# Performance work log

Hardware: AMD Instinct MI355X
Metric: run time of the kernel (lower is better)

Reference implementation:

```python
import jax, jax.numpy as jnp
import numpy as np

V, D, H, F, L, SMAX = 32000, 768, 12, 3072, 6, 512
DN = D // H
NEG = -1e9
EPS = 1e-5


def _pos_encoding(S, d, dtype):
    # pe[pos,2i]   = sin(pos / 10000**(2i/d))
    # pe[pos,2i+1] = cos(pos / 10000**(2(i+1)/d))   (note the i+1, as in source)
    pos = jnp.arange(S, dtype=jnp.float32)[:, None]
    i = jnp.arange(d // 2, dtype=jnp.float32)[None, :]
    pe_sin = jnp.sin(pos / jnp.power(10000.0, 2.0 * i / d))
    pe_cos = jnp.cos(pos / jnp.power(10000.0, 2.0 * (i + 1.0) / d))
    pe = jnp.zeros((S, d), jnp.float32)
    pe = pe.at[:, 0::2].set(pe_sin).at[:, 1::2].set(pe_cos)
    return pe.astype(dtype)


def _layernorm(z, g, b):
    m = jnp.mean(z, axis=-1, keepdims=True)
    v = jnp.mean(jnp.square(z - m), axis=-1, keepdims=True)
    return (z - m) * jax.lax.rsqrt(v + EPS) * g + b


def setup_inputs() -> dict:
    key = jax.random.key(0)
    ks = jax.random.split(key, 20)
    s = 0.02
    inp = {
        "x": jax.random.randint(ks[0], (16, 512), 0, V, dtype=jnp.int64 if jax.config.read("jax_enable_x64") else jnp.int32),
        "padding_mask": jax.random.randint(ks[1], (16, 512, 512), 0, 2, dtype=jnp.int32),
        "emb": jax.random.normal(ks[2], (V, D), jnp.float32) * s,
        # per-head separate projections, stacked: [L, H, D, DN]
        "Wq": jax.random.normal(ks[3], (L, H, D, DN), jnp.float32) * s,
        "bq": jnp.zeros((L, H, DN), jnp.float32),
        "Wk": jax.random.normal(ks[4], (L, H, D, DN), jnp.float32) * s,
        "bk": jnp.zeros((L, H, DN), jnp.float32),
        "Wv": jax.random.normal(ks[5], (L, H, D, DN), jnp.float32) * s,
        "bv": jnp.zeros((L, H, DN), jnp.float32),
        "Wo": jax.random.normal(ks[6], (L, D, D), jnp.float32) * s,
        "bo": jnp.zeros((L, D), jnp.float32),
        "W1": jax.random.normal(ks[7], (L, D, F), jnp.float32) * s,
        "b1": jnp.zeros((L, F), jnp.float32),
        "W2": jax.random.normal(ks[8], (L, F, D), jnp.float32) * s,
        "b2": jnp.zeros((L, D), jnp.float32),
        "g1": jnp.ones((L, D), jnp.float32),
        "be1": jnp.zeros((L, D), jnp.float32),
        "g2": jnp.ones((L, D), jnp.float32),
        "be2": jnp.zeros((L, D), jnp.float32),
    }
    return inp


def reference(x, padding_mask, emb, Wq, bq, Wk, bk, Wv, bv, Wo, bo,
              W1, b1, W2, b2, g1, be1, g2, be2):
    B, S = x.shape
    h = emb[x]                                   # [B,S,D]
    h = h + _pos_encoding(S, D, h.dtype)[None]   # dropout is identity in eval
    bias = padding_mask.astype(h.dtype)[:, None] * NEG   # [B,1,S,S]
    scale = 1.0 / np.sqrt(DN)
    for l in range(L):
        q = jnp.einsum("bsd,hde->bhse", h, Wq[l]) + bq[l][None, :, None, :]
        k = jnp.einsum("bsd,hde->bhse", h, Wk[l]) + bk[l][None, :, None, :]
        v = jnp.einsum("bsd,hde->bhse", h, Wv[l]) + bv[l][None, :, None, :]
        scores = jnp.einsum("bhse,bhte->bhst", q, k) * scale + bias
        attn = jax.nn.softmax(scores, axis=-1)
        o = jnp.einsum("bhst,bhte->bhse", attn, v)        # [B,H,S,DN]
        o = o.transpose(0, 2, 1, 3).reshape(B, S, D)      # concat heads
        o = o @ Wo[l] + bo[l]
        h = _layernorm(h + o, g1[l], be1[l])
        ff = jax.nn.relu(h @ W1[l] + b1[l]) @ W2[l] + b2[l]
        h = _layernorm(h + ff, g2[l], be2[l])
    return h
```

## Files before the change

### kernel.cpp

```cpp
#include <hip/hip_runtime.h>
#include <hip/hip_bf16.h>
#include <math.h>

#define B_  16
#define S_  512
#define D_  768
#define H_  12
#define DN_ 64
#define F_  3072
#define L_  6
#define T_  (B_*S_)
#define QKVN 2304
#define TDC ((size_t)T_*D_)

typedef unsigned short ushort_t;
typedef short short8 __attribute__((ext_vector_type(8)));
typedef float floatx4 __attribute__((ext_vector_type(4)));

#define LDS_AS(p) ((__attribute__((address_space(3))) void*)(p))
#define GLB_AS(p) ((const __attribute__((address_space(1))) void*)(p))

static __device__ __forceinline__ float b2f(ushort_t u) {
  union { unsigned int i; float f; } x; x.i = ((unsigned int)u) << 16; return x.f;
}
static __device__ __forceinline__ ushort_t f2b(float f) {
  union { float f; unsigned int i; } x; x.f = f;
  unsigned int r = x.i + 0x7fffu + ((x.i >> 16) & 1u);
  return (ushort_t)(r >> 16);
}

__global__ __launch_bounds__(64) void probe_x(const int* __restrict__ x,
                                              int* __restrict__ xstride) {
  if (threadIdx.x == 0) {
    int allzero = 1;
    for (int i = 0; i < 64; ++i) allzero &= (x[2 * i + 1] == 0) ? 1 : 0;
    *xstride = allzero ? 2 : 1;
  }
}

__global__ __launch_bounds__(256) void pe_kernel(float* __restrict__ pe) {
  const int s = blockIdx.x;
  const float pos = (float)s;
  for (int d = threadIdx.x; d < D_; d += 256) {
    float v;
    if ((d & 1) == 0) {
      float freq = powf(10000.0f, -(float)d * (1.0f / 768.0f));
      v = sinf(pos * freq);
    } else {
      float freq = powf(10000.0f, -(float)(d + 1) * (1.0f / 768.0f));
      v = cosf(pos * freq);
    }
    pe[(size_t)s * D_ + d] = v;
  }
}

__global__ __launch_bounds__(256) void embed_pe(const int* __restrict__ x,
                                                const int* __restrict__ xstride,
                                                const float* __restrict__ emb,
                                                const float* __restrict__ pe,
                                                float* __restrict__ h32,
                                                ushort_t* __restrict__ h16) {
  const int t = blockIdx.x;
  const int s = t & (S_ - 1);
  const int tok = x[t * (*xstride)];
  const float* ep = emb + (size_t)tok * D_;
  const float* pp = pe + (size_t)s * D_;
  for (int d = threadIdx.x; d < D_; d += 256) {
    float v = ep[d] + pp[d];
    h32[(size_t)t * D_ + d] = v;
    h16[(size_t)t * D_ + d] = f2b(v);
  }
}

__global__ __launch_bounds__(256) void mask_bits(const int* __restrict__ mask,
                                                 unsigned long long* __restrict__ bits) {
  const int gw = (blockIdx.x * 256 + threadIdx.x) >> 6;
  const int lane = threadIdx.x & 63;
  const int m = mask[(size_t)gw * 64 + lane];
  unsigned long long bal = __ballot(m != 0);
  if (lane == 0) bits[gw] = bal;
}

__global__ __launch_bounds__(256) void pack_bias(const float* __restrict__ bq,
                                                 const float* __restrict__ bk,
                                                 const float* __restrict__ bv,
                                                 float* __restrict__ bqkv) {
  const int i = blockIdx.x * 256 + threadIdx.x;
  if (i < L_ * D_) {
    const int l = i / D_, c = i - l * D_;
    bqkv[(size_t)l * QKVN + c]          = bq[i];
    bqkv[(size_t)l * QKVN + 768 + c]    = bk[i];
    bqkv[(size_t)l * QKVN + 1536 + c]   = bv[i];
  }
}

__global__ __launch_bounds__(256) void transpose_cast(const float* __restrict__ in,
                                                      ushort_t* __restrict__ out,
                                                      int R, int C, int ZH,
                                                      size_t strideL, size_t strideH) {
  __shared__ float tb[32][33];
  const int c0 = blockIdx.x * 32, r0 = blockIdx.y * 32;
  const int z = blockIdx.z;
  const float* ib = in + (size_t)z * R * C;
  ushort_t* ob = out + (size_t)(z / ZH) * strideL + (size_t)(z % ZH) * strideH;
  const int i = threadIdx.x >> 5;
  const int j = threadIdx.x & 31;
  #pragma unroll
  for (int t = 0; t < 4; ++t)
    tb[i + 8 * t][j] = ib[(size_t)(r0 + i + 8 * t) * C + c0 + j];
  __syncthreads();
  #pragma unroll
  for (int t = 0; t < 4; ++t)
    ob[(size_t)(c0 + i + 8 * t) * R + r0 + j] = f2b(tb[j][i + 8 * t]);
}

__global__ __launch_bounds__(256) void transpose_v(const ushort_t* __restrict__ qkv,
                                                   ushort_t* __restrict__ vT) {
  __shared__ ushort_t tb[32][33];
  const int s0 = blockIdx.x * 32, e0 = blockIdx.y * 32;
  const int bh = blockIdx.z;
  const int b = bh / 12, hh = bh - b * 12;
  const int i = threadIdx.x >> 5, j = threadIdx.x & 31;
  #pragma unroll
  for (int t = 0; t < 4; ++t)
    tb[i + 8 * t][j] = qkv[((size_t)(b * S_ + s0 + i + 8 * t)) * QKVN + 1536 + hh * 64 + e0 + j];
  __syncthreads();
  #pragma unroll
  for (int t = 0; t < 4; ++t)
    vT[((size_t)(bh * 64 + e0 + i + 8 * t)) * S_ + s0 + j] = tb[j][i + 8 * t];
}

template<int RELU>
__global__ __launch_bounds__(256) void gemm_mfma(const ushort_t* __restrict__ A,
                                                 const ushort_t* __restrict__ Bt,
                                                 const float* __restrict__ bias,
                                                 ushort_t* __restrict__ C,
                                                 int N, int K) {
  __shared__ ushort_t Alds[128 * 64];
  __shared__ ushort_t Blds[128 * 64];
  const int tid = threadIdx.x;
  const int lane = tid & 63, wave = tid >> 6;
  const int l16 = lane & 15, quad = lane >> 4;
  const int m0 = (wave >> 1) * 64, n0 = (wave & 1) * 64;
  const int nb = gridDim.x;
  const int flat = blockIdx.y * nb + blockIdx.x;
  const int grp = flat / (8 * nb);
  const int rem = flat - grp * 8 * nb;
  const int bm = (grp * 8 + (rem & 7)) * 128;
  const int bn = (rem >> 3) * 128;
  const int r0 = tid >> 3;
  const int ch = tid & 7;
  const int koff = (ch ^ (r0 & 7)) * 8;

  const ushort_t* ga = A  + (size_t)(bm + r0) * K + koff;
  const ushort_t* gb = Bt + (size_t)(bn + r0) * K + koff;
  ushort_t* la = &Alds[tid * 8];
  ushort_t* lb = &Blds[tid * 8];
  const int swz = l16 & 7;

  floatx4 acc[4][4] = {};
  for (int k0 = 0; k0 < K; k0 += 64) {
    __syncthreads();
    #pragma unroll
    for (int j = 0; j < 4; ++j) {
      __builtin_amdgcn_global_load_lds(GLB_AS(ga + k0 + (size_t)(j * 32) * K), LDS_AS(la + j * 2048), 16, 0, 0);
      __builtin_amdgcn_global_load_lds(GLB_AS(gb + k0 + (size_t)(j * 32) * K), LDS_AS(lb + j * 2048), 16, 0, 0);
    }
    __syncthreads();
    #pragma unroll
    for (int kk = 0; kk < 2; ++kk) {
      short8 af[4], bf[4];
      #pragma unroll
      for (int fi = 0; fi < 4; ++fi) {
        const int row = m0 + fi * 16 + l16;
        af[fi] = *(const short8*)&Alds[row * 64 + ((((kk << 2) + quad) ^ swz) * 8)];
      }
      #pragma unroll
      for (int fj = 0; fj < 4; ++fj) {
        const int row = n0 + fj * 16 + l16;
        bf[fj] = *(const short8*)&Blds[row * 64 + ((((kk << 2) + quad) ^ swz) * 8)];
      }
      #pragma unroll
      for (int fi = 0; fi < 4; ++fi)
        #pragma unroll
        for (int fj = 0; fj < 4; ++fj)
          acc[fi][fj] = __builtin_amdgcn_mfma_f32_16x16x32_bf16(af[fi], bf[fj], acc[fi][fj], 0, 0, 0);
    }
  }
  #pragma unroll
  for (int fi = 0; fi < 4; ++fi) {
    #pragma unroll
    for (int fj = 0; fj < 4; ++fj) {
      const int row = bm + m0 + fi * 16 + quad * 4;
      const int col = bn + n0 + fj * 16 + l16;
      const float bv = bias[col];
      #pragma unroll
      for (int r = 0; r < 4; ++r) {
        float v = acc[fi][fj][r] + bv;
        if (RELU) v = fmaxf(v, 0.0f);
        C[(size_t)(row + r) * N + col] = f2b(v);
      }
    }
  }
}

__global__ __launch_bounds__(256) void gemm_mfma_sk(const ushort_t* __restrict__ A,
                                                    const ushort_t* __restrict__ Bt,
                                                    const float* __restrict__ bias,
                                                    ushort_t* __restrict__ P,
                                                    int N, int K) {
  __shared__ ushort_t Alds[128 * 64];
  __shared__ ushort_t Blds[128 * 64];
  const int tid = threadIdx.x;
  const int lane = tid & 63, wave = tid >> 6;
  const int l16 = lane & 15, quad = lane >> 4;
  const int m0 = (wave >> 1) * 64, n0 = (wave & 1) * 64;
  const int nb = gridDim.x;
  const int flat = blockIdx.y * nb + blockIdx.x;
  const int grp = flat / (8 * nb);
  const int rem = flat - grp * 8 * nb;
  const int bm = (grp * 8 + (rem & 7)) * 128;
  const int bn = (rem >> 3) * 128;
  const int r0 = tid >> 3;
  const int ch = tid & 7;
  const int koff = (ch ^ (r0 & 7)) * 8;
  const int z = blockIdx.z;
  const int Kh = K >> 1;

  const ushort_t* ga = A  + (size_t)(bm + r0) * K + (size_t)z * Kh + koff;
  const ushort_t* gb = Bt + (size_t)(bn + r0) * K + (size_t)z * Kh + koff;
  ushort_t* la = &Alds[tid * 8];
  ushort_t* lb = &Blds[tid * 8];
  ushort_t* Pz = P + (size_t)z * T_ * N;
  const int swz = l16 & 7;

  floatx4 acc[4][4] = {};
  for (int k0 = 0; k0 < Kh; k0 += 64) {
    __syncthreads();
    #pragma unroll
    for (int j = 0; j < 4; ++j) {
      __builtin_amdgcn_global_load_lds(GLB_AS(ga + k0 + (size_t)(j * 32) * K), LDS_AS(la + j * 2048), 16, 0, 0);
      __builtin_amdgcn_global_load_lds(GLB_AS(gb + k0 + (size_t)(j * 32) * K), LDS_AS(lb + j * 2048), 16, 0, 0);
    }
    __syncthreads();
    #pragma unroll
    for (int kk = 0; kk < 2; ++kk) {
      short8 af[4], bf[4];
      #pragma unroll
      for (int fi = 0; fi < 4; ++fi) {
        const int row = m0 + fi * 16 + l16;
        af[fi] = *(const short8*)&Alds[row * 64 + ((((kk << 2) + quad) ^ swz) * 8)];
      }
      #pragma unroll
      for (int fj = 0; fj < 4; ++fj) {
        const int row = n0 + fj * 16 + l16;
        bf[fj] = *(const short8*)&Blds[row * 64 + ((((kk << 2) + quad) ^ swz) * 8)];
      }
      #pragma unroll
      for (int fi = 0; fi < 4; ++fi)
        #pragma unroll
        for (int fj = 0; fj < 4; ++fj)
          acc[fi][fj] = __builtin_amdgcn_mfma_f32_16x16x32_bf16(af[fi], bf[fj], acc[fi][fj], 0, 0, 0);
    }
  }
  #pragma unroll
  for (int fi = 0; fi < 4; ++fi) {
    #pragma unroll
    for (int fj = 0; fj < 4; ++fj) {
      const int row = bm + m0 + fi * 16 + quad * 4;
      const int col = bn + n0 + fj * 16 + l16;
      const float bv = (z == 0) ? bias[col] : 0.0f;
      #pragma unroll
      for (int r = 0; r < 4; ++r) {
        float v = acc[fi][fj][r] + bv;
        Pz[(size_t)(row + r) * N + col] = f2b(v);
      }
    }
  }
}

__global__ __launch_bounds__(256) void attn_mfma(const ushort_t* __restrict__ qkv,
                                                 const ushort_t* __restrict__ vT,
                                                 const unsigned long long* __restrict__ mbits,
                                                 ushort_t* __restrict__ o) {
  __shared__ ushort_t Qs[64][72];
  __shared__ ushort_t Ks[64][72];
  __shared__ ushort_t Vt[64][72];
  __shared__ ushort_t Ps[64][72];
  const int F = blockIdx.x;
  const int xcd = F & 7;
  const int sfl = F >> 3;
  const int qt = sfl & 7;
  const int gg = sfl >> 3;
  const int bh = gg * 8 + xcd;
  const int b = bh / 12, hh = bh - b * 12;
  const int tid = threadIdx.x;
  const int lane = tid & 63, w = tid >> 6;
  const int l16 = lane & 15, quad = lane >> 4;

  for (int c = tid; c < 1024; c += 256) {
    const int row = c >> 4, e0 = (c & 15) * 4;
    *(ushort4*)&Qs[row][e0] =
        *(const ushort4*)(qkv + ((size_t)(b * S_ + qt * 64 + row)) * QKVN + hh * 64 + e0);
  }

  floatx4 Oa[4] = {};
  float lrow[4] = {};
  const ushort_t* vbase = vT + ((size_t)(b * H_ + hh) * 64) * S_;

  ushort4 kreg[4], vreg[4];
  #pragma unroll
  for (int i = 0; i < 4; ++i) {
    const int c = tid + i * 256;
    const int row = c >> 4, e0 = (c & 15) * 4;
    kreg[i] = *(const ushort4*)(qkv + ((size_t)(b * S_ + row)) * QKVN + 768 + hh * 64 + e0);
    vreg[i] = *(const ushort4*)(vbase + (size_t)row * S_ + e0);
  }

  for (int kt = 0; kt < 8; ++kt) {
    __syncthreads();
    #pragma unroll
    for (int i = 0; i < 4; ++i) {
      const int c = tid + i * 256;
      const int row = c >> 4, e0 = (c & 15) * 4;
      *(ushort4*)&Ks[row][e0] = kreg[i];
      *(ushort4*)&Vt[row][e0] = vreg[i];
    }
    if (kt < 7) {
      #pragma unroll
      for (int i = 0; i < 4; ++i) {
        const int c = tid + i * 256;
        const int row = c >> 4, e0 = (c & 15) * 4;
        kreg[i] = *(const ushort4*)(qkv + ((size_t)(b * S_ + (kt + 1) * 64 + row)) * QKVN + 768 + hh * 64 + e0);
        vreg[i] = *(const ushort4*)(vbase + (size_t)row * S_ + (kt + 1) * 64 + e0);
      }
    }
    __syncthreads();

    floatx4 sa[4] = {};
    __builtin_amdgcn_s_setprio(1);
    #pragma unroll
    for (int st = 0; st < 2; ++st) {
      short8 aq = *(const short8*)&Qs[w * 16 + l16][st * 32 + quad * 8];
      #pragma unroll
      for (int fj = 0; fj < 4; ++fj) {
        short8 bk = *(const short8*)&Ks[fj * 16 + l16][st * 32 + quad * 8];
        sa[fj] = __builtin_amdgcn_mfma_f32_16x16x32_bf16(aq, bk, sa[fj], 0, 0, 0);
      }
    }
    __builtin_amdgcn_s_setprio(0);

    #pragma unroll
    for (int r = 0; r < 4; ++r) {
      const int qrow = qt * 64 + w * 16 + quad * 4 + r;
      const unsigned long long m64 = mbits[((size_t)(b * S_ + qrow) << 3) + kt];
      float p0 = __expf(fmaf(sa[0][r], 0.125f, ((m64 >> l16) & 1ull)        ? -1e9f : -16.0f));
      float p1 = __expf(fmaf(sa[1][r], 0.125f, ((m64 >> (16 + l16)) & 1ull) ? -1e9f : -16.0f));
      float p2 = __expf(fmaf(sa[2][r], 0.125f, ((m64 >> (32 + l16)) & 1ull) ? -1e9f : -16.0f));
      float p3 = __expf(fmaf(sa[3][r], 0.125f, ((m64 >> (48 + l16)) & 1ull) ? -1e9f : -16.0f));
      const int prow = w * 16 + quad * 4 + r;
      Ps[prow][ 0 + l16] = f2b(p0);
      Ps[prow][16 + l16] = f2b(p1);
      Ps[prow][32 + l16] = f2b(p2);
      Ps[prow][48 + l16] = f2b(p3);
      lrow[r] += (p0 + p1) + (p2 + p3);
    }

    __builtin_amdgcn_s_setprio(1);
    #pragma unroll
    for (int st = 0; st < 2; ++st) {
      short8 ap = *(const short8*)&Ps[w * 16 + l16][st * 32 + quad * 8];
      #pragma unroll
      for (int fe = 0; fe < 4; ++fe) {
        short8 bv = *(const short8*)&Vt[fe * 16 + l16][st * 32 + quad * 8];
        Oa[fe] = __builtin_amdgcn_mfma_f32_16x16x32_bf16(ap, bv, Oa[fe], 0, 0, 0);
      }
    }
    __builtin_amdgcn_s_setprio(0);
  }

  #pragma unroll
  for (int r = 0; r < 4; ++r) {
    float rs = lrow[r];
    rs += __shfl_xor(rs, 1); rs += __shfl_xor(rs, 2);
    rs += __shfl_xor(rs, 4); rs += __shfl_xor(rs, 8);
    const float inv = 1.0f / rs;
    const size_t tok = (size_t)(b * S_ + qt * 64 + w * 16 + quad * 4 + r);
    #pragma unroll
    for (int fe = 0; fe < 4; ++fe)
      o[tok * D_ + hh * 64 + fe * 16 + l16] = f2b(Oa[fe][r] * inv);
  }
}

__global__ __launch_bounds__(256) void add_ln(float* __restrict__ h,
                                              const ushort_t* __restrict__ r,
                                              const float* __restrict__ g,
                                              const float* __restrict__ be,
                                              ushort_t* __restrict__ h16) {
  const int t = blockIdx.x;
  const int tid = threadIdx.x;
  __shared__ float red[8];
  const size_t base = (size_t)t * D_;
  float x0 = h[base + tid]       + b2f(r[base + tid])       + b2f(r[TDC + base + tid]);
  float x1 = h[base + tid + 256] + b2f(r[base + tid + 256]) + b2f(r[TDC + base + tid + 256]);
  float x2 = h[base + tid + 512] + b2f(r[base + tid + 512]) + b2f(r[TDC + base + tid + 512]);
  float s = x0 + x1 + x2;
  #pragma unroll
  for (int off = 32; off > 0; off >>= 1) s += __shfl_down(s, off);
  if ((tid & 63) == 0) red[tid >> 6] = s;
  __syncthreads();
  if (tid == 0) red[4] = (red[0] + red[1] + red[2] + red[3]) * (1.0f / 768.0f);
  __syncthreads();
  const float m = red[4];
  float d0 = x0 - m, d1 = x1 - m, d2 = x2 - m;
  float s2 = d0 * d0 + d1 * d1 + d2 * d2;
  #pragma unroll
  for (int off = 32; off > 0; off >>= 1) s2 += __shfl_down(s2, off);
  if ((tid & 63) == 0) red[tid >> 6] = s2;
  __syncthreads();
  if (tid == 0) red[5] = (red[0] + red[1] + red[2] + red[3]) * (1.0f / 768.0f);
  __syncthreads();
  const float rs = rsqrtf(red[5] + 1e-5f);
  float y0 = d0 * rs * g[tid]       + be[tid];
  float y1 = d1 * rs * g[tid + 256] + be[tid + 256];
  float y2 = d2 * rs * g[tid + 512] + be[tid + 512];
  h[base + tid]       = y0; h16[base + tid]       = f2b(y0);
  h[base + tid + 256] = y1; h16[base + tid + 256] = f2b(y1);
  h[base + tid + 512] = y2; h16[base + tid + 512] = f2b(y2);
}

__global__ __launch_bounds__(256) void write_out(const float* __restrict__ h,
                                                 float* __restrict__ out, int n) {
  int i = blockIdx.x * 256 + threadIdx.x;
  if (i < n) out[i] = h[i];
}

extern "C" void kernel_launch(void* const* d_in, const int* in_sizes, int n_in,
                              void* d_out, int out_size, void* d_ws, size_t ws_size,
                              hipStream_t stream) {
  (void)in_sizes; (void)n_in; (void)out_size; (void)ws_size;
  const int* x    = (const int*)d_in[0];
  const int* mask = (const int*)d_in[1];
  const float* emb = (const float*)d_in[2];
  const float* Wq  = (const float*)d_in[3];
  const float* bq  = (const float*)d_in[4];
  const float* Wk  = (const float*)d_in[5];
  const float* bk  = (const float*)d_in[6];
  const float* Wv  = (const float*)d_in[7];
  const float* bv  = (const float*)d_in[8];
  const float* Wo  = (const float*)d_in[9];
  const float* bo  = (const float*)d_in[10];
  const float* W1  = (const float*)d_in[11];
  const float* b1  = (const float*)d_in[12];
  const float* W2  = (const float*)d_in[13];
  const float* b2  = (const float*)d_in[14];
  const float* g1  = (const float*)d_in[15];
  const float* be1 = (const float*)d_in[16];
  const float* g2  = (const float*)d_in[17];
  const float* be2 = (const float*)d_in[18];

  const size_t TD  = TDC;
  const size_t DD  = (size_t)D_ * D_;
  const size_t WDD = (size_t)L_ * DD;
  const size_t WDF = (size_t)L_ * D_ * F_;

  float* h32 = (float*)d_ws;
  ushort_t* h16  = (ushort_t*)(h32 + TD);
  ushort_t* qkv16 = h16 + TD;
  ushort_t* o1   = qkv16 + 3 * TD;
  ushort_t* o2   = o1 + TD;
  ushort_t* ff   = qkv16;
  ushort_t* vT   = o2 + TD;
  ushort_t* bias16 = vT + TD;
  ushort_t* WqkvT = bias16 + (size_t)B_ * S_ * S_;
  ushort_t* WoT  = WqkvT + 3 * WDD;
  ushort_t* W1T  = WoT + WDD;
  ushort_t* W2T  = W1T + WDF;
  float* bqkv    = (float*)(W2T + WDF);
  int* xstride   = (int*)(bqkv + (size_t)L_ * QKVN);
  float* pe32    = (float*)o1;
  unsigned long long* mbits = (unsigned long long*)bias16;

  probe_x<<<dim3(1), 64, 0, stream>>>(x, xstride);
  pe_kernel<<<dim3(S_), 256, 0, stream>>>(pe32);
  transpose_cast<<<dim3(2, 24, 72), 256, 0, stream>>>(Wq, WqkvT,          768, 64, 12, 3 * DD, (size_t)64 * 768);
  transpose_cast<<<dim3(2, 24, 72), 256, 0, stream>>>(Wk, WqkvT + DD,     768, 64, 12, 3 * DD, (size_t)64 * 768);
  transpose_cast<<<dim3(2, 24, 72), 256, 0, stream>>>(Wv, WqkvT + 2 * DD, 768, 64, 12, 3 * DD, (size_t)64 * 768);
  transpose_cast<<<dim3(24, 24, 6), 256, 0, stream>>>(Wo, WoT, 768, 768, 1, DD, 0);
  transpose_cast<<<dim3(96, 24, 6), 256, 0, stream>>>(W1, W1T, 768, 3072, 1, (size_t)D_ * F_, 0);
  transpose_cast<<<dim3(24, 96, 6), 256, 0, stream>>>(W2, W2T, 3072, 768, 1, (size_t)D_ * F_, 0);
  pack_bias<<<dim3((L_ * D_ + 255) / 256), 256, 0, stream>>>(bq, bk, bv, bqkv);
  mask_bits<<<dim3((B_ * S_ * S_) / 256), 256, 0, stream>>>(mask, mbits);
  embed_pe<<<dim3(T_), 256, 0, stream>>>(x, xstride, emb, pe32, h32, h16);

  const dim3 gQKV(QKVN / 128, T_ / 128);
  const dim3 gDsk(D_ / 128, T_ / 128, 2);
  const dim3 gF(F_ / 128, T_ / 128);
  for (int l = 0; l < L_; ++l) {
    const size_t oDD = (size_t)l * DD;
    const size_t oDF = (size_t)l * D_ * F_;
    gemm_mfma<0><<<gQKV, 256, 0, stream>>>(h16, WqkvT + (size_t)l * 3 * DD, bqkv + (size_t)l * QKVN, qkv16, QKVN, D_);
    transpose_v<<<dim3(16, 2, B_ * H_), 256, 0, stream>>>(qkv16, vT);
    attn_mfma<<<dim3(8 * H_ * B_), 256, 0, stream>>>(qkv16, vT, mbits, o1);
    gemm_mfma_sk<<<gDsk, 256, 0, stream>>>(o1, WoT + oDD, bo + l * D_, o2, D_, D_);
    add_ln<<<dim3(T_), 256, 0, stream>>>(h32, o2, g1 + l * D_, be1 + l * D_, h16);
    gemm_mfma<1><<<gF, 256, 0, stream>>>(h16, W1T + oDF, b1 + l * F_, ff, F_, D_);
    gemm_mfma_sk<<<gDsk, 256, 0, stream>>>(ff, W2T + oDF, b2 + l * D_, o2, D_, F_);
    add_ln<<<dim3(T_), 256, 0, stream>>>(h32, o2, g2 + l * D_, be2 + l * D_, h16);
  }
  write_out<<<dim3((unsigned)(TD / 256)), 256, 0, stream>>>(h32, (float*)d_out, (int)TD);
}
```

Baseline: 1.823 ms.

## Double-buffer LDS tiles in MFMA GEMM kernels to overlap loads with compute

Both GEMM kernels (plain and split-K) now keep two LDS buffers for A and B tiles. The next K-tile is prefetched with global_load_lds while MFMAs run on the current one, and one barrier per iteration replaces two. This targets the exposed global-load latency in the main loop. In exchange, LDS use doubles to 64KB per block, which may cut occupancy. The single barrier also relies on the vmcnt wait it implies to make the async LDS writes visible.

```diff
diff --git a/kernel.cpp b/kernel.cpp
--- a/kernel.cpp
+++ b/kernel.cpp
@@ -136,8 +136,8 @@
                                                  const float* __restrict__ bias,
                                                  ushort_t* __restrict__ C,
                                                  int N, int K) {
-  __shared__ ushort_t Alds[128 * 64];
-  __shared__ ushort_t Blds[128 * 64];
+  __shared__ ushort_t Alds[2][128 * 64];
+  __shared__ ushort_t Blds[2][128 * 64];
   const int tid = threadIdx.x;
   const int lane = tid & 63, wave = tid >> 6;
   const int l16 = lane & 15, quad = lane >> 4;
@@ -154,31 +154,40 @@
 
   const ushort_t* ga = A  + (size_t)(bm + r0) * K + koff;
   const ushort_t* gb = Bt + (size_t)(bn + r0) * K + koff;
-  ushort_t* la = &Alds[tid * 8];
-  ushort_t* lb = &Blds[tid * 8];
+  const int ldst = tid * 8;
   const int swz = l16 & 7;
+  const int NT = K >> 6;
 
   floatx4 acc[4][4] = {};
-  for (int k0 = 0; k0 < K; k0 += 64) {
-    __syncthreads();
-    #pragma unroll
-    for (int j = 0; j < 4; ++j) {
-      __builtin_amdgcn_global_load_lds(GLB_AS(ga + k0 + (size_t)(j * 32) * K), LDS_AS(la + j * 2048), 16, 0, 0);
-      __builtin_amdgcn_global_load_lds(GLB_AS(gb + k0 + (size_t)(j * 32) * K), LDS_AS(lb + j * 2048), 16, 0, 0);
-    }
-    __syncthreads();
+  #pragma unroll
+  for (int j = 0; j < 4; ++j) {
+    __builtin_amdgcn_global_load_lds(GLB_AS(ga + (size_t)(j * 32) * K), LDS_AS(&Alds[0][ldst + j * 2048]), 16, 0, 0);
+    __builtin_amdgcn_global_load_lds(GLB_AS(gb + (size_t)(j * 32) * K), LDS_AS(&Blds[0][ldst + j * 2048]), 16, 0, 0);
+  }
+  __syncthreads();
+
+  int cur = 0;
+  for (int t = 0; t < NT; ++t) {
+    if (t + 1 < NT) {
+      const int k0 = (t + 1) << 6;
+      #pragma unroll
+      for (int j = 0; j < 4; ++j) {
+        __builtin_amdgcn_global_load_lds(GLB_AS(ga + k0 + (size_t)(j * 32) * K), LDS_AS(&Alds[cur ^ 1][ldst + j * 2048]), 16, 0, 0);
+        __builtin_amdgcn_global_load_lds(GLB_AS(gb + k0 + (size_t)(j * 32) * K), LDS_AS(&Blds[cur ^ 1][ldst + j * 2048]), 16, 0, 0);
+      }
+    }
     #pragma unroll
     for (int kk = 0; kk < 2; ++kk) {
       short8 af[4], bf[4];
       #pragma unroll
       for (int fi = 0; fi < 4; ++fi) {
         const int row = m0 + fi * 16 + l16;
-        af[fi] = *(const short8*)&Alds[row * 64 + ((((kk << 2) + quad) ^ swz) * 8)];
+        af[fi] = *(const short8*)&Alds[cur][row * 64 + ((((kk << 2) + quad) ^ swz) * 8)];
       }
       #pragma unroll
       for (int fj = 0; fj < 4; ++fj) {
         const int row = n0 + fj * 16 + l16;
-        bf[fj] = *(const short8*)&Blds[row * 64 + ((((kk << 2) + quad) ^ swz) * 8)];
+        bf[fj] = *(const short8*)&Blds[cur][row * 64 + ((((kk << 2) + quad) ^ swz) * 8)];
       }
       #pragma unroll
       for (int fi = 0; fi < 4; ++fi)
@@ -186,6 +195,8 @@
         for (int fj = 0; fj < 4; ++fj)
           acc[fi][fj] = __builtin_amdgcn_mfma_f32_16x16x32_bf16(af[fi], bf[fj], acc[fi][fj], 0, 0, 0);
     }
+    __syncthreads();
+    cur ^= 1;
   }
   #pragma unroll
   for (int fi = 0; fi < 4; ++fi) {
@@ -209,8 +220,8 @@
                                                     const float* __restrict__ bias,
                                                     ushort_t* __restrict__ P,
                                                     int N, int K) {
-  __shared__ ushort_t Alds[128 * 64];
-  __shared__ ushort_t Blds[128 * 64];
+  __shared__ ushort_t Alds[2][128 * 64];
+  __shared__ ushort_t Blds[2][128 * 64];
   const int tid = threadIdx.x;
   const int lane = tid & 63, wave = tid >> 6;
   const int l16 = lane & 15, quad = lane >> 4;
@@ -229,32 +240,41 @@
 
   const ushort_t* ga = A  + (size_t)(bm + r0) * K + (size_t)z * Kh + koff;
   const ushort_t* gb = Bt + (size_t)(bn + r0) * K + (size_t)z * Kh + koff;
-  ushort_t* la = &Alds[tid * 8];
-  ushort_t* lb = &Blds[tid * 8];
   ushort_t* Pz = P + (size_t)z * T_ * N;
+  const int ldst = tid * 8;
   const int swz = l16 & 7;
+  const int NT = Kh >> 6;
 
   floatx4 acc[4][4] = {};
-  for (int k0 = 0; k0 < Kh; k0 += 64) {
-    __syncthreads();
-    #pragma unroll
-    for (int j = 0; j < 4; ++j) {
-      __builtin_amdgcn_global_load_lds(GLB_AS(ga + k0 + (size_t)(j * 32) * K), LDS_AS(la + j * 2048), 16, 0, 0);
-      __builtin_amdgcn_global_load_lds(GLB_AS(gb + k0 + (size_t)(j * 32) * K), LDS_AS(lb + j * 2048), 16, 0, 0);
-    }
-    __syncthreads();
+  #pragma unroll
+  for (int j = 0; j < 4; ++j) {
+    __builtin_amdgcn_global_load_lds(GLB_AS(ga + (size_t)(j * 32) * K), LDS_AS(&Alds[0][ldst + j * 2048]), 16, 0, 0);
+    __builtin_amdgcn_global_load_lds(GLB_AS(gb + (size_t)(j * 32) * K), LDS_AS(&Blds[0][ldst + j * 2048]), 16, 0, 0);
+  }
+  __syncthreads();
+
+  int cur = 0;
+  for (int t = 0; t < NT; ++t) {
+    if (t + 1 < NT) {
+      const int k0 = (t + 1) << 6;
+      #pragma unroll
+      for (int j = 0; j < 4; ++j) {
+        __builtin_amdgcn_global_load_lds(GLB_AS(ga + k0 + (size_t)(j * 32) * K), LDS_AS(&Alds[cur ^ 1][ldst + j * 2048]), 16, 0, 0);
+        __builtin_amdgcn_global_load_lds(GLB_AS(gb + k0 + (size_t)(j * 32) * K), LDS_AS(&Blds[cur ^ 1][ldst + j * 2048]), 16, 0, 0);
+      }
+    }
     #pragma unroll
     for (int kk = 0; kk < 2; ++kk) {
       short8 af[4], bf[4];
       #pragma unroll
       for (int fi = 0; fi < 4; ++fi) {
         const int row = m0 + fi * 16 + l16;
-        af[fi] = *(const short8*)&Alds[row * 64 + ((((kk << 2) + quad) ^ swz) * 8)];
+        af[fi] = *(const short8*)&Alds[cur][row * 64 + ((((kk << 2) + quad) ^ swz) * 8)];
       }
       #pragma unroll
       for (int fj = 0; fj < 4; ++fj) {
         const int row = n0 + fj * 16 + l16;
-        bf[fj] = *(const short8*)&Blds[row * 64 + ((((kk << 2) + quad) ^ swz) * 8)];
+        bf[fj] = *(const short8*)&Blds[cur][row * 64 + ((((kk << 2) + quad) ^ swz) * 8)];
       }
       #pragma unroll
       for (int fi = 0; fi < 4; ++fi)
@@ -262,6 +282,8 @@
         for (int fj = 0; fj < 4; ++fj)
           acc[fi][fj] = __builtin_amdgcn_mfma_f32_16x16x32_bf16(af[fi], bf[fj], acc[fi][fj], 0, 0, 0);
     }
+    __syncthreads();
+    cur ^= 1;
   }
   #pragma unroll
   for (int fi = 0; fi < 4; ++fi) {
```

Result: slower. 1.933 ms (+6.0%).
